# Kernel tuning notes

Hardware: AMD Instinct MI355X
Metric: run time of the kernel (lower is better)

Reference implementation:

```python
import jax, jax.numpy as jnp
import numpy as np

H, C, HID, NLAYERS, B = 4, 32, 128, 3, 2048
EPS = 1e-5


def _gat_layer(x, src, dst, n, W, b, a_src, a_dst):
    # x: [N, HID]; W: [HID, H*C]; a_src/a_dst: [H, C]
    h = (x @ W).reshape(n, H, C)                      # [N,H,C]
    s_src = jnp.einsum('nhc,hc->nh', h, a_src)        # [N,H]
    s_dst = jnp.einsum('nhc,hc->nh', h, a_dst)
    e = jax.nn.leaky_relu(s_src[src] + s_dst[dst], 0.2)   # [E,H]
    m = jax.ops.segment_max(e, dst, num_segments=n)
    p = jnp.exp(e - m[dst])
    z = jax.ops.segment_sum(p, dst, num_segments=n)
    alpha = p / z[dst]                                 # scatter-softmax over in-edges
    msg = h[src] * alpha[:, :, None]                   # [E,H,C]
    out = jax.ops.segment_sum(msg, dst, num_segments=n)
    return out.reshape(n, H * C) + b


def _layernorm(x, g, bta):
    mu = jnp.mean(x, axis=-1, keepdims=True)
    var = jnp.mean(jnp.square(x - mu), axis=-1, keepdims=True)
    return (x - mu) * jax.lax.rsqrt(var + EPS) * g + bta


def _encode(x, edge_index, batch, W_in, b_in, Wg, bg, att_src, att_dst, ln_gamma, ln_beta):
    n = x.shape[0]
    # add self loops (PyG GATConv default)
    loops = jnp.arange(n, dtype=edge_index.dtype)
    src = jnp.concatenate([edge_index[0], loops])
    dst = jnp.concatenate([edge_index[1], loops])
    h = jax.nn.relu(x @ W_in + b_in)
    for i in range(NLAYERS):
        res = h
        h = _gat_layer(h, src, dst, n, Wg[i], bg[i], att_src[i], att_dst[i])
        h = _layernorm(h, ln_gamma[i], ln_beta[i])
        h = jax.nn.relu(h)
        h = h + res
    # global mean pool
    sums = jax.ops.segment_sum(h, batch, num_segments=B)
    cnt = jax.ops.segment_sum(jnp.ones((n,), h.dtype), batch, num_segments=B)
    return sums / jnp.maximum(cnt, 1.0)[:, None]


def setup_inputs() -> dict:
    key = jax.random.key(0)
    ks = jax.random.split(key, 24)
    Nt, Et, Np, Ep, D = 131072, 2097152, 24576, 196608, 480
    inp = {}
    inp['tcr_x'] = jax.random.normal(ks[0], (Nt, D), jnp.float32)
    inp['tcr_edge_index'] = jax.random.randint(ks[1], (2, Et), 0, Nt)
    inp['tcr_batch'] = jnp.sort(jax.random.randint(ks[2], (Nt,), 0, B))
    inp['pep_x'] = jax.random.normal(ks[3], (Np, D), jnp.float32)
    inp['pep_edge_index'] = jax.random.randint(ks[4], (2, Ep), 0, Np)
    inp['pep_batch'] = jnp.sort(jax.random.randint(ks[5], (Np,), 0, B))
    s_in = 1.0 / np.sqrt(D)
    inp['W_in'] = jax.random.normal(ks[6], (D, HID), jnp.float32) * s_in
    inp['b_in'] = jnp.zeros((HID,), jnp.float32)
    s_h = 1.0 / np.sqrt(HID)
    inp['Wg'] = jax.random.normal(ks[7], (NLAYERS, HID, H * C), jnp.float32) * s_h
    inp['bg'] = jnp.zeros((NLAYERS, HID), jnp.float32)
    inp['att_src'] = jax.random.normal(ks[8], (NLAYERS, H, C), jnp.float32) * (1.0 / np.sqrt(C))
    inp['att_dst'] = jax.random.normal(ks[9], (NLAYERS, H, C), jnp.float32) * (1.0 / np.sqrt(C))
    inp['ln_gamma'] = jnp.ones((NLAYERS, HID), jnp.float32)
    inp['ln_beta'] = jnp.zeros((NLAYERS, HID), jnp.float32)
    inp['Wc1'] = jax.random.normal(ks[10], (2 * HID, HID), jnp.float32) * (1.0 / np.sqrt(2 * HID))
    inp['bc1'] = jnp.zeros((HID,), jnp.float32)
    inp['Wc2'] = jax.random.normal(ks[11], (HID, HID // 2), jnp.float32) * s_h
    inp['bc2'] = jnp.zeros((HID // 2,), jnp.float32)
    inp['Wc3'] = jax.random.normal(ks[12], (HID // 2, 1), jnp.float32) * (1.0 / np.sqrt(HID // 2))
    inp['bc3'] = jnp.zeros((1,), jnp.float32)
    return inp


def reference(tcr_x, tcr_edge_index, tcr_batch, pep_x, pep_edge_index, pep_batch,
              W_in, b_in, Wg, bg, att_src, att_dst, ln_gamma, ln_beta,
              Wc1, bc1, Wc2, bc2, Wc3, bc3):
    tcr = _encode(tcr_x, tcr_edge_index, tcr_batch, W_in, b_in, Wg, bg, att_src, att_dst, ln_gamma, ln_beta)
    pep = _encode(pep_x, pep_edge_index, pep_batch, W_in, b_in, Wg, bg, att_src, att_dst, ln_gamma, ln_beta)
    z = jnp.concatenate([tcr, pep], axis=1)            # [B, 256]
    z = jax.nn.relu(z @ Wc1 + bc1)
    z = jax.nn.relu(z @ Wc2 + bc2)
    return jax.nn.sigmoid(z @ Wc3 + bc3)               # [B, 1]
```

## Files before the change

### kernel.cpp

```cpp
#include <hip/hip_runtime.h>
#include <hip/hip_fp16.h>
#include <math.h>

#define NHEAD   4
#define CDIM    32
#define HIDDIM  128
#define NLAYERS 3
#define DIN     480
#define LN_EPS  1e-5f
#define NSPLIT  4

typedef _Float16 f16x8 __attribute__((ext_vector_type(8)));
typedef float    f32x4 __attribute__((ext_vector_type(4)));
typedef int      int4u __attribute__((ext_vector_type(4), aligned(4)));

__global__ void hist_kernel(const int* __restrict__ tei, const int* __restrict__ pei,
                            int* __restrict__ deg, int Et, int Ep, int Nt, int N) {
    int i = blockIdx.x * 256 + threadIdx.x;
    int tot = Et + Ep + N;
    if (i >= tot) return;
    int d;
    if (i < Et)            d = tei[Et + i];
    else if (i < Et + Ep)  d = pei[Ep + (i - Et)] + Nt;
    else                   d = i - Et - Ep;
    atomicAdd(&deg[d], 1);
}

__global__ __launch_bounds__(256) void fill_kernel(const int* __restrict__ tei,
                                                   const int* __restrict__ pei,
                                                   int* __restrict__ cursor,
                                                   int* __restrict__ col,
                                                   int Et, int Ep, int Nt, int N,
                                                   float oscale) {
    int oid    = blockIdx.x & (NSPLIT - 1);
    int chunk  = blockIdx.x / NSPLIT;
    int nchunk = gridDim.x / NSPLIT;
    int tot = Et + Ep + N;
    int per = (tot + nchunk - 1) / nchunk;
    int e0 = chunk * per;
    int e1 = min(e0 + per, tot);
    for (int i = e0 + (int)threadIdx.x; i < e1; i += 256) {
        int d;
        bool self = false;
        if (i < Et)           d = tei[Et + i];
        else if (i < Et + Ep) d = pei[Ep + (i - Et)] + Nt;
        else                { d = i - Et - Ep; self = true; }
        int owner = (int)((float)d * oscale);
        owner = owner > NSPLIT - 1 ? NSPLIT - 1 : owner;
        if (owner != oid) continue;
        int s;
        if (self)        s = d;
        else if (i < Et) s = tei[i];
        else             s = pei[i - Et] + Nt;
        int pos = atomicAdd(&cursor[d], 1);
        col[pos] = s;
    }
}

__global__ __launch_bounds__(256) void scan_reduce(const int* __restrict__ deg,
                                                   int* __restrict__ part, int N) {
    __shared__ int sm[256];
    int t = threadIdx.x;
    int base = blockIdx.x * 1024 + t * 4;
    int4 v = make_int4(0, 0, 0, 0);
    if (base + 3 < N) v = *(const int4*)(deg + base);
    else if (base < N) {
        v.x = deg[base];
        if (base + 1 < N) v.y = deg[base + 1];
        if (base + 2 < N) v.z = deg[base + 2];
    }
    sm[t] = v.x + v.y + v.z + v.w;
    __syncthreads();
    for (int off = 128; off >= 1; off >>= 1) {
        if (t < off) sm[t] += sm[t + off];
        __syncthreads();
    }
    if (t == 0) part[blockIdx.x] = sm[0];
}

__global__ __launch_bounds__(256) void scan_partials(int* __restrict__ part,
                                                     int* __restrict__ rowptr,
                                                     int npart, int N) {
    __shared__ int sm[256];
    int t = threadIdx.x;
    sm[t] = (t < npart) ? part[t] : 0;
    __syncthreads();
    for (int off = 1; off < 256; off <<= 1) {
        int u = (t >= off) ? sm[t - off] : 0;
        __syncthreads();
        sm[t] += u;
        __syncthreads();
    }
    if (t < npart) part[t] = (t == 0) ? 0 : sm[t - 1];
    if (t == 0) rowptr[N] = sm[255];
}

__global__ __launch_bounds__(256) void scan_final(const int* __restrict__ deg,
                                                  const int* __restrict__ part,
                                                  int* __restrict__ rowptr,
                                                  int* __restrict__ cursor, int N) {
    __shared__ int sm[256];
    int t = threadIdx.x;
    int base = blockIdx.x * 1024 + t * 4;
    int4 v = make_int4(0, 0, 0, 0);
    if (base + 3 < N) v = *(const int4*)(deg + base);
    else if (base < N) {
        v.x = deg[base];
        if (base + 1 < N) v.y = deg[base + 1];
        if (base + 2 < N) v.z = deg[base + 2];
    }
    sm[t] = v.x + v.y + v.z + v.w;
    __syncthreads();
    for (int off = 1; off < 256; off <<= 1) {
        int u = (t >= off) ? sm[t - off] : 0;
        __syncthreads();
        sm[t] += u;
        __syncthreads();
    }
    int run = ((t == 0) ? 0 : sm[t - 1]) + part[blockIdx.x];
    if (base < N)     { rowptr[base]     = run; cursor[base]     = run; run += v.x; }
    if (base + 1 < N) { rowptr[base + 1] = run; cursor[base + 1] = run; run += v.y; }
    if (base + 2 < N) { rowptr[base + 2] = run; cursor[base + 2] = run; run += v.z; }
    if (base + 3 < N) { rowptr[base + 3] = run; cursor[base + 3] = run; }
}

__global__ void transpose_w(const float* __restrict__ W, _Float16* __restrict__ Wt,
                            int K) {
    int idx = blockIdx.x * 256 + threadIdx.x;
    if (idx >= K * 128) return;
    int n = idx / K, k = idx - n * K;
    Wt[idx] = (_Float16)W[(size_t)k * 128 + n];
}

#define ASTRIDE 40

template<int OUT_F16>
__global__ __launch_bounds__(256) void mfma_gemm(const float* __restrict__ A,
                                                 const _Float16* __restrict__ Wt,
                                                 const float* __restrict__ bias,
                                                 void* __restrict__ Cout,
                                                 const float* __restrict__ a_src,
                                                 const float* __restrict__ a_dst,
                                                 float* __restrict__ ssrc,
                                                 float* __restrict__ sdst,
                                                 int K) {
    __shared__ _Float16 As[64 * ASTRIDE];
    __shared__ _Float16 Ws[128 * ASTRIDE];
    const int tid  = threadIdx.x;
    const int bn   = blockIdx.x * 64;
    const int wave = tid >> 6, lane = tid & 63;
    const int lm   = lane & 15, q = lane >> 4;

    f32x4 acc[8];
#pragma unroll
    for (int i = 0; i < 8; ++i) acc[i] = (f32x4){0.f, 0.f, 0.f, 0.f};

    for (int kt = 0; kt < K; kt += 32) {
#pragma unroll
        for (int p = 0; p < 2; ++p) {
            int f  = p * 256 + tid;
            int r  = f >> 3;
            int c4 = (f & 7) * 4;
            float4 v = *(const float4*)(A + (size_t)(bn + r) * K + kt + c4);
            _Float16* d = &As[r * ASTRIDE + c4];
            d[0] = (_Float16)v.x; d[1] = (_Float16)v.y;
            d[2] = (_Float16)v.z; d[3] = (_Float16)v.w;
        }
#pragma unroll
        for (int p = 0; p < 2; ++p) {
            int f   = p * 256 + tid;
            int n   = f >> 2;
            int seg = (f & 3) * 8;
            *(float4*)(&Ws[n * ASTRIDE + seg]) =
                *(const float4*)(Wt + (size_t)n * K + kt + seg);
        }
        __syncthreads();
        f16x8 af = *(const f16x8*)(&As[(wave * 16 + lm) * ASTRIDE + q * 8]);
#pragma unroll
        for (int nt = 0; nt < 8; ++nt) {
            f16x8 bf = *(const f16x8*)(&Ws[(nt * 16 + lm) * ASTRIDE + q * 8]);
            acc[nt] = __builtin_amdgcn_mfma_f32_16x16x32_f16(af, bf, acc[nt], 0, 0, 0);
        }
        __syncthreads();
    }

    const int row0 = bn + wave * 16 + q * 4;
    if (OUT_F16) {
        _Float16* C = (_Float16*)Cout;
        float as[8], ad[8];
#pragma unroll
        for (int nt = 0; nt < 8; ++nt) {
            as[nt] = a_src[nt * 16 + lm];
            ad[nt] = a_dst[nt * 16 + lm];
        }
        float myS = 0.f, myD = 0.f;
#pragma unroll
        for (int i = 0; i < 4; ++i) {
            float ps[4], pd[4];
#pragma unroll
            for (int h = 0; h < 4; ++h) {
                ps[h] = as[2 * h] * acc[2 * h][i] + as[2 * h + 1] * acc[2 * h + 1][i];
                pd[h] = ad[2 * h] * acc[2 * h][i] + ad[2 * h + 1] * acc[2 * h + 1][i];
            }
#pragma unroll
            for (int k = 1; k < 16; k <<= 1) {
#pragma unroll
                for (int h = 0; h < 4; ++h) {
                    ps[h] += __shfl_xor(ps[h], k, 16);
                    pd[h] += __shfl_xor(pd[h], k, 16);
                }
            }
            if ((lm >> 2) == i) { myS = ps[lm & 3]; myD = pd[lm & 3]; }
#pragma unroll
            for (int nt = 0; nt < 8; ++nt)
                C[(size_t)(row0 + i) * 128 + nt * 16 + lm] = (_Float16)acc[nt][i];
        }
        int sr = (row0 + (lm >> 2)) * 4 + (lm & 3);
        ssrc[sr] = myS;
        sdst[sr] = myD;
    } else {
        float* C = (float*)Cout;
#pragma unroll
        for (int nt = 0; nt < 8; ++nt) {
            int c = nt * 16 + lm;
            float bv = bias[c];
#pragma unroll
            for (int i = 0; i < 4; ++i)
                C[(size_t)(row0 + i) * 128 + c] = fmaxf(acc[nt][i] + bv, 0.f);
        }
    }
}

__global__ __launch_bounds__(256) void gather_kernel(const f16x8* __restrict__ h2v,
                                                     const float* __restrict__ ssrc,
                                                     const float* __restrict__ sdst,
                                                     const int* __restrict__ rowptr,
                                                     const int* __restrict__ col,
                                                     const float* __restrict__ bg,
                                                     const float* __restrict__ gamma,
                                                     const float* __restrict__ beta,
                                                     float* __restrict__ hio, int N) {
    int wave = threadIdx.x >> 6, lane = threadIdx.x & 63;
    int g = lane >> 4, t = lane & 15;
    int n = blockIdx.x * 16 + wave * 4 + g;
    bool valid = n < N;
    int nn = valid ? n : 0;
    int head = t >> 2;
    int beg = rowptr[nn];
    int end = valid ? rowptr[nn + 1] : beg;
    float sd = sdst[nn * 4 + head];

    float m = -1e30f, z = 0.f;
    float a[8];
#pragma unroll
    for (int k = 0; k < 8; ++k) a[k] = 0.f;

    int j = beg;
    for (; j + 3 < end; j += 4) {
        int4u cv = *(const int4u*)(col + j);
        int s0 = cv.x, s1 = cv.y, s2 = cv.z, s3 = cv.w;
        float e0 = ssrc[s0 * 4 + head] + sd;
        float e1 = ssrc[s1 * 4 + head] + sd;
        float e2 = ssrc[s2 * 4 + head] + sd;
        float e3 = ssrc[s3 * 4 + head] + sd;
        f16x8 v0 = h2v[(size_t)s0 * 16 + t];
        f16x8 v1 = h2v[(size_t)s1 * 16 + t];
        f16x8 v2 = h2v[(size_t)s2 * 16 + t];
        f16x8 v3 = h2v[(size_t)s3 * 16 + t];
        e0 = fmaxf(e0, 0.2f * e0);
        e1 = fmaxf(e1, 0.2f * e1);
        e2 = fmaxf(e2, 0.2f * e2);
        e3 = fmaxf(e3, 0.2f * e3);
        float nm = fmaxf(fmaxf(fmaxf(e0, e1), fmaxf(e2, e3)), m);
        float r  = __expf(m - nm);
        m = nm;
        float p0 = __expf(e0 - nm);
        float p1 = __expf(e1 - nm);
        float p2 = __expf(e2 - nm);
        float p3 = __expf(e3 - nm);
        z = z * r + (p0 + p1 + p2 + p3);
#pragma unroll
        for (int k = 0; k < 8; ++k) a[k] *= r;
#pragma unroll
        for (int k = 0; k < 8; ++k) a[k] = fmaf((float)v0[k], p0, a[k]);
#pragma unroll
        for (int k = 0; k < 8; ++k) a[k] = fmaf((float)v1[k], p1, a[k]);
#pragma unroll
        for (int k = 0; k < 8; ++k) a[k] = fmaf((float)v2[k], p2, a[k]);
#pragma unroll
        for (int k = 0; k < 8; ++k) a[k] = fmaf((float)v3[k], p3, a[k]);
    }
    for (; j < end; ++j) {
        int s = col[j];
        float e = ssrc[s * 4 + head] + sd;
        e = fmaxf(e, 0.2f * e);
        f16x8 v = h2v[(size_t)s * 16 + t];
        float nm = fmaxf(m, e);
        float r  = __expf(m - nm);
        float p  = __expf(e - nm);
        m = nm;
        z = z * r + p;
#pragma unroll
        for (int k = 0; k < 8; ++k) a[k] = fmaf((float)v[k], p, a[k] * r);
    }

    if (!valid) return;
    float inv = 1.f / z;
    int c0 = t * 8;
    float4 bgv0 = *(const float4*)(bg + c0);
    float4 bgv1 = *(const float4*)(bg + c0 + 4);
    float o[8];
    o[0] = a[0] * inv + bgv0.x; o[1] = a[1] * inv + bgv0.y;
    o[2] = a[2] * inv + bgv0.z; o[3] = a[3] * inv + bgv0.w;
    o[4] = a[4] * inv + bgv1.x; o[5] = a[5] * inv + bgv1.y;
    o[6] = a[6] * inv + bgv1.z; o[7] = a[7] * inv + bgv1.w;
    float s = 0.f;
#pragma unroll
    for (int k = 0; k < 8; ++k) s += o[k];
#pragma unroll
    for (int k = 1; k < 16; k <<= 1) s += __shfl_xor(s, k, 16);
    float mu = s * (1.f / 128.f);
    float q = 0.f;
#pragma unroll
    for (int k = 0; k < 8; ++k) q += (o[k] - mu) * (o[k] - mu);
#pragma unroll
    for (int k = 1; k < 16; k <<= 1) q += __shfl_xor(q, k, 16);
    float rs = rsqrtf(q * (1.f / 128.f) + LN_EPS);
    float4 gm0 = *(const float4*)(gamma + c0);
    float4 gm1 = *(const float4*)(gamma + c0 + 4);
    float4 bt0 = *(const float4*)(beta + c0);
    float4 bt1 = *(const float4*)(beta + c0 + 4);
    float* hrow = hio + (size_t)n * 128 + c0;
    float4 r0 = *(const float4*)(hrow);
    float4 r1 = *(const float4*)(hrow + 4);
    float4 y0, y1;
    y0.x = fmaxf((o[0] - mu) * rs * gm0.x + bt0.x, 0.f) + r0.x;
    y0.y = fmaxf((o[1] - mu) * rs * gm0.y + bt0.y, 0.f) + r0.y;
    y0.z = fmaxf((o[2] - mu) * rs * gm0.z + bt0.z, 0.f) + r0.z;
    y0.w = fmaxf((o[3] - mu) * rs * gm0.w + bt0.w, 0.f) + r0.w;
    y1.x = fmaxf((o[4] - mu) * rs * gm1.x + bt1.x, 0.f) + r1.x;
    y1.y = fmaxf((o[5] - mu) * rs * gm1.y + bt1.y, 0.f) + r1.y;
    y1.z = fmaxf((o[6] - mu) * rs * gm1.z + bt1.z, 0.f) + r1.z;
    y1.w = fmaxf((o[7] - mu) * rs * gm1.w + bt1.w, 0.f) + r1.w;
    *(float4*)(hrow)     = y0;
    *(float4*)(hrow + 4) = y1;
}

__global__ __launch_bounds__(128) void pool_kernel(const float* __restrict__ h,
                                                   const int* __restrict__ tb,
                                                   const int* __restrict__ pb,
                                                   float* __restrict__ pooled,
                                                   int Nt, int Np, int B) {
    int blk = blockIdx.x;
    bool is_t = blk < B;
    int bb = is_t ? blk : blk - B;
    const int* __restrict__ arr = is_t ? tb : pb;
    int len  = is_t ? Nt : Np;
    int base = is_t ? 0 : Nt;
    int off  = is_t ? 0 : 128;
    int lo = 0, hi = len;
    while (lo < hi) { int mid = (lo + hi) >> 1; if (arr[mid] < bb) lo = mid + 1; else hi = mid; }
    int beg = lo;
    hi = len;
    while (lo < hi) { int mid = (lo + hi) >> 1; if (arr[mid] < bb + 1) lo = mid + 1; else hi = mid; }
    int end = lo;
    int t = threadIdx.x;
    float a0 = 0.f, a1 = 0.f, a2 = 0.f, a3 = 0.f;
    int n = beg;
    for (; n + 3 < end; n += 4) {
        a0 += h[(size_t)(base + n)     * 128 + t];
        a1 += h[(size_t)(base + n + 1) * 128 + t];
        a2 += h[(size_t)(base + n + 2) * 128 + t];
        a3 += h[(size_t)(base + n + 3) * 128 + t];
    }
    for (; n < end; ++n) a0 += h[(size_t)(base + n) * 128 + t];
    float s = (a0 + a1) + (a2 + a3);
    float invc = 1.f / (float)max(end - beg, 1);
    pooled[(size_t)bb * 256 + off + t] = s * invc;
}

__global__ __launch_bounds__(128) void classifier_kernel(const float* __restrict__ pooled,
                                                         const float* __restrict__ Wc1,
                                                         const float* __restrict__ bc1,
                                                         const float* __restrict__ Wc2,
                                                         const float* __restrict__ bc2,
                                                         const float* __restrict__ Wc3,
                                                         const float* __restrict__ bc3,
                                                         float* __restrict__ outp, int B) {
    __shared__ float z[256];
    __shared__ float a1[128];
    __shared__ float a2[64];
    int r = blockIdx.x, t = threadIdx.x;
    z[t]       = pooled[(size_t)r * 256 + t];
    z[128 + t] = pooled[(size_t)r * 256 + 128 + t];
    __syncthreads();
    float acc = bc1[t];
    for (int k = 0; k < 256; ++k) acc = fmaf(z[k], Wc1[k * 128 + t], acc);
    a1[t] = fmaxf(acc, 0.f);
    __syncthreads();
    if (t < 64) {
        float a = bc2[t];
        for (int k = 0; k < 128; ++k) a = fmaf(a1[k], Wc2[k * 64 + t], a);
        a2[t] = fmaxf(a, 0.f);
    }
    __syncthreads();
    if (t < 64) {
        float p = a2[t] * Wc3[t];
#pragma unroll
        for (int k = 1; k < 64; k <<= 1) p += __shfl_xor(p, k);
        if (t == 0) outp[r] = 1.f / (1.f + __expf(-(p + bc3[0])));
    }
}

extern "C" void kernel_launch(void* const* d_in, const int* in_sizes, int n_in,
                              void* d_out, int out_size, void* d_ws, size_t ws_size,
                              hipStream_t stream) {
    const float* tcr_x     = (const float*)d_in[0];
    const int*   tcr_ei    = (const int*)d_in[1];
    const int*   tcr_batch = (const int*)d_in[2];
    const float* pep_x     = (const float*)d_in[3];
    const int*   pep_ei    = (const int*)d_in[4];
    const int*   pep_batch = (const int*)d_in[5];
    const float* W_in      = (const float*)d_in[6];
    const float* b_in      = (const float*)d_in[7];
    const float* Wg        = (const float*)d_in[8];
    const float* bg        = (const float*)d_in[9];
    const float* att_src   = (const float*)d_in[10];
    const float* att_dst   = (const float*)d_in[11];
    const float* ln_gamma  = (const float*)d_in[12];
    const float* ln_beta   = (const float*)d_in[13];
    const float* Wc1       = (const float*)d_in[14];
    const float* bc1       = (const float*)d_in[15];
    const float* Wc2       = (const float*)d_in[16];
    const float* bc2       = (const float*)d_in[17];
    const float* Wc3       = (const float*)d_in[18];
    const float* bc3       = (const float*)d_in[19];

    const int Nt = in_sizes[0] / DIN;
    const int Et = in_sizes[1] / 2;
    const int Np = in_sizes[3] / DIN;
    const int Ep = in_sizes[4] / 2;
    const int B  = out_size;
    const int N  = Nt + Np;
    const int Etot = Et + Ep + N;

    char* w = (char*)d_ws;
    size_t o = 0;
    auto alloc = [&](size_t bytes) -> char* {
        size_t r = (o + 255) & ~(size_t)255;
        o = r + bytes;
        return w + r;
    };
    float*    pooled = (float*)alloc((size_t)B * 256 * 4);
    float*    h_a    = (float*)alloc((size_t)N * 128 * 4);
    _Float16* h2h    = (_Float16*)alloc((size_t)N * 128 * 2);
    _Float16* WtIn   = (_Float16*)alloc((size_t)128 * DIN * 2);
    _Float16* WtG    = (_Float16*)alloc((size_t)NLAYERS * 128 * 128 * 2);
    float*    ssrc   = (float*)alloc((size_t)N * 4 * 4);
    float*    sdst   = (float*)alloc((size_t)N * 4 * 4);
    int* rowptr      = (int*)alloc((size_t)(N + 1) * 4);
    int* cursor      = (int*)alloc((size_t)N * 4);
    int* deg         = (int*)alloc((size_t)N * 4);
    int* part        = (int*)alloc(256 * 4);
    int* col         = (int*)alloc((size_t)Etot * 4);
    (void)ws_size; (void)n_in;

    hipMemsetAsync(deg, 0, (size_t)N * 4, stream);

    transpose_w<<<(128 * DIN + 255) / 256, 256, 0, stream>>>(W_in, WtIn, DIN);
    for (int i = 0; i < NLAYERS; ++i)
        transpose_w<<<(128 * 128 + 255) / 256, 256, 0, stream>>>(
            Wg + (size_t)i * HIDDIM * HIDDIM, WtG + (size_t)i * 128 * 128, 128);

    hist_kernel<<<(Etot + 255) / 256, 256, 0, stream>>>(tcr_ei, pep_ei, deg, Et, Ep, Nt, N);
    int nblk = (N + 1023) / 1024;
    scan_reduce<<<nblk, 256, 0, stream>>>(deg, part, N);
    scan_partials<<<1, 256, 0, stream>>>(part, rowptr, nblk, N);
    scan_final<<<nblk, 256, 0, stream>>>(deg, part, rowptr, cursor, N);
    fill_kernel<<<NSPLIT * 512, 256, 0, stream>>>(tcr_ei, pep_ei, cursor, col,
                                                  Et, Ep, Nt, N, (float)NSPLIT / (float)N);

    mfma_gemm<0><<<Nt / 64, 256, 0, stream>>>(tcr_x, WtIn, b_in, h_a,
                                              nullptr, nullptr, nullptr, nullptr, DIN);
    mfma_gemm<0><<<Np / 64, 256, 0, stream>>>(pep_x, WtIn, b_in, h_a + (size_t)Nt * 128,
                                              nullptr, nullptr, nullptr, nullptr, DIN);

    for (int i = 0; i < NLAYERS; ++i) {
        mfma_gemm<1><<<N / 64, 256, 0, stream>>>(h_a, WtG + (size_t)i * 128 * 128,
                                                 nullptr, h2h,
                                                 att_src + i * NHEAD * CDIM,
                                                 att_dst + i * NHEAD * CDIM,
                                                 ssrc, sdst, 128);
        gather_kernel<<<(N + 15) / 16, 256, 0, stream>>>((const f16x8*)h2h, ssrc, sdst,
                                                         rowptr, col, bg + i * HIDDIM,
                                                         ln_gamma + i * HIDDIM,
                                                         ln_beta + i * HIDDIM, h_a, N);
    }
    pool_kernel<<<2 * B, 128, 0, stream>>>(h_a, tcr_batch, pep_batch, pooled, Nt, Np, B);

    classifier_kernel<<<B, 128, 0, stream>>>(pooled, Wc1, bc1, Wc2, bc2,
                                             Wc3, bc3, (float*)d_out, B);
}
```

Measured before the change: 1.148 ms.

## Merge launches and software-pipeline gather loads in GAT aggregation

After: 1.149 ms. No clear change (+0.1%).

```diff
diff --git a/kernel.cpp b/kernel.cpp
--- a/kernel.cpp
+++ b/kernel.cpp
@@ -124,18 +124,31 @@
     if (base + 3 < N) { rowptr[base + 3] = run; cursor[base + 3] = run; }
 }
 
-__global__ void transpose_w(const float* __restrict__ W, _Float16* __restrict__ Wt,
-                            int K) {
+__global__ __launch_bounds__(256) void transpose_all(const float* __restrict__ W_in,
+                                                     const float* __restrict__ Wg,
+                                                     _Float16* __restrict__ WtIn,
+                                                     _Float16* __restrict__ WtG) {
     int idx = blockIdx.x * 256 + threadIdx.x;
-    if (idx >= K * 128) return;
-    int n = idx / K, k = idx - n * K;
-    Wt[idx] = (_Float16)W[(size_t)k * 128 + n];
+    const int NIN = 128 * DIN;
+    if (idx < NIN) {
+        int n = idx / DIN, k = idx - n * DIN;
+        WtIn[idx] = (_Float16)W_in[(size_t)k * 128 + n];
+    } else {
+        int r = idx - NIN;
+        if (r >= NLAYERS * 128 * 128) return;
+        int l = r / (128 * 128), rr = r - l * 128 * 128;
+        int n = rr >> 7, k = rr & 127;
+        WtG[(size_t)l * 128 * 128 + rr] =
+            (_Float16)Wg[(size_t)l * 128 * 128 + (size_t)k * 128 + n];
+    }
 }
 
 #define ASTRIDE 40
 
 template<int OUT_F16>
 __global__ __launch_bounds__(256) void mfma_gemm(const float* __restrict__ A,
+                                                 const float* __restrict__ A2,
+                                                 int NtRows,
                                                  const _Float16* __restrict__ Wt,
                                                  const float* __restrict__ bias,
                                                  void* __restrict__ Cout,
@@ -151,6 +164,11 @@
     const int wave = tid >> 6, lane = tid & 63;
     const int lm   = lane & 15, q = lane >> 4;
 
+    const float* __restrict__ Abase;
+    int arow;
+    if (A2 && bn >= NtRows) { Abase = A2; arow = bn - NtRows; }
+    else                    { Abase = A;  arow = bn; }
+
     f32x4 acc[8];
 #pragma unroll
     for (int i = 0; i < 8; ++i) acc[i] = (f32x4){0.f, 0.f, 0.f, 0.f};
@@ -161,7 +179,7 @@
             int f  = p * 256 + tid;
             int r  = f >> 3;
             int c4 = (f & 7) * 4;
-            float4 v = *(const float4*)(A + (size_t)(bn + r) * K + kt + c4);
+            float4 v = *(const float4*)(Abase + (size_t)(arow + r) * K + kt + c4);
             _Float16* d = &As[r * ASTRIDE + c4];
             d[0] = (_Float16)v.x; d[1] = (_Float16)v.y;
             d[2] = (_Float16)v.z; d[3] = (_Float16)v.w;
@@ -255,22 +273,12 @@
 #pragma unroll
     for (int k = 0; k < 8; ++k) a[k] = 0.f;
 
-    int j = beg;
-    for (; j + 3 < end; j += 4) {
-        int4u cv = *(const int4u*)(col + j);
-        int s0 = cv.x, s1 = cv.y, s2 = cv.z, s3 = cv.w;
-        float e0 = ssrc[s0 * 4 + head] + sd;
-        float e1 = ssrc[s1 * 4 + head] + sd;
-        float e2 = ssrc[s2 * 4 + head] + sd;
-        float e3 = ssrc[s3 * 4 + head] + sd;
-        f16x8 v0 = h2v[(size_t)s0 * 16 + t];
-        f16x8 v1 = h2v[(size_t)s1 * 16 + t];
-        f16x8 v2 = h2v[(size_t)s2 * 16 + t];
-        f16x8 v3 = h2v[(size_t)s3 * 16 + t];
-        e0 = fmaxf(e0, 0.2f * e0);
-        e1 = fmaxf(e1, 0.2f * e1);
-        e2 = fmaxf(e2, 0.2f * e2);
-        e3 = fmaxf(e3, 0.2f * e3);
+    auto compute4 = [&](f16x8 v0, f16x8 v1, f16x8 v2, f16x8 v3,
+                        float x0, float x1, float x2, float x3) {
+        float e0 = x0 + sd; e0 = fmaxf(e0, 0.2f * e0);
+        float e1 = x1 + sd; e1 = fmaxf(e1, 0.2f * e1);
+        float e2 = x2 + sd; e2 = fmaxf(e2, 0.2f * e2);
+        float e3 = x3 + sd; e3 = fmaxf(e3, 0.2f * e3);
         float nm = fmaxf(fmaxf(fmaxf(e0, e1), fmaxf(e2, e3)), m);
         float r  = __expf(m - nm);
         m = nm;
@@ -289,6 +297,37 @@
         for (int k = 0; k < 8; ++k) a[k] = fmaf((float)v2[k], p2, a[k]);
 #pragma unroll
         for (int k = 0; k < 8; ++k) a[k] = fmaf((float)v3[k], p3, a[k]);
+    };
+
+    int j = beg;
+    int nch = (end - beg) >> 2;
+    if (nch > 0) {
+        int4u cv = *(const int4u*)(col + j);
+        f16x8 v0 = h2v[(size_t)cv.x * 16 + t];
+        f16x8 v1 = h2v[(size_t)cv.y * 16 + t];
+        f16x8 v2 = h2v[(size_t)cv.z * 16 + t];
+        f16x8 v3 = h2v[(size_t)cv.w * 16 + t];
+        float x0 = ssrc[cv.x * 4 + head];
+        float x1 = ssrc[cv.y * 4 + head];
+        float x2 = ssrc[cv.z * 4 + head];
+        float x3 = ssrc[cv.w * 4 + head];
+        for (int c = 1; c < nch; ++c) {
+            j += 4;
+            int4u cn = *(const int4u*)(col + j);
+            f16x8 w0 = h2v[(size_t)cn.x * 16 + t];
+            f16x8 w1 = h2v[(size_t)cn.y * 16 + t];
+            f16x8 w2 = h2v[(size_t)cn.z * 16 + t];
+            f16x8 w3 = h2v[(size_t)cn.w * 16 + t];
+            float u0 = ssrc[cn.x * 4 + head];
+            float u1 = ssrc[cn.y * 4 + head];
+            float u2 = ssrc[cn.z * 4 + head];
+            float u3 = ssrc[cn.w * 4 + head];
+            compute4(v0, v1, v2, v3, x0, x1, x2, x3);
+            v0 = w0; v1 = w1; v2 = w2; v3 = w3;
+            x0 = u0; x1 = u1; x2 = u2; x3 = u3;
+        }
+        compute4(v0, v1, v2, v3, x0, x1, x2, x3);
+        j += 4;
     }
     for (; j < end; ++j) {
         int s = col[j];
@@ -346,53 +385,55 @@
     *(float4*)(hrow + 4) = y1;
 }
 
-__global__ __launch_bounds__(128) void pool_kernel(const float* __restrict__ h,
-                                                   const int* __restrict__ tb,
-                                                   const int* __restrict__ pb,
-                                                   float* __restrict__ pooled,
-                                                   int Nt, int Np, int B) {
-    int blk = blockIdx.x;
-    bool is_t = blk < B;
-    int bb = is_t ? blk : blk - B;
-    const int* __restrict__ arr = is_t ? tb : pb;
-    int len  = is_t ? Nt : Np;
-    int base = is_t ? 0 : Nt;
-    int off  = is_t ? 0 : 128;
-    int lo = 0, hi = len;
-    while (lo < hi) { int mid = (lo + hi) >> 1; if (arr[mid] < bb) lo = mid + 1; else hi = mid; }
-    int beg = lo;
-    hi = len;
-    while (lo < hi) { int mid = (lo + hi) >> 1; if (arr[mid] < bb + 1) lo = mid + 1; else hi = mid; }
-    int end = lo;
-    int t = threadIdx.x;
-    float a0 = 0.f, a1 = 0.f, a2 = 0.f, a3 = 0.f;
-    int n = beg;
-    for (; n + 3 < end; n += 4) {
-        a0 += h[(size_t)(base + n)     * 128 + t];
-        a1 += h[(size_t)(base + n + 1) * 128 + t];
-        a2 += h[(size_t)(base + n + 2) * 128 + t];
-        a3 += h[(size_t)(base + n + 3) * 128 + t];
-    }
-    for (; n < end; ++n) a0 += h[(size_t)(base + n) * 128 + t];
-    float s = (a0 + a1) + (a2 + a3);
-    float invc = 1.f / (float)max(end - beg, 1);
-    pooled[(size_t)bb * 256 + off + t] = s * invc;
-}
-
-__global__ __launch_bounds__(128) void classifier_kernel(const float* __restrict__ pooled,
-                                                         const float* __restrict__ Wc1,
-                                                         const float* __restrict__ bc1,
-                                                         const float* __restrict__ Wc2,
-                                                         const float* __restrict__ bc2,
-                                                         const float* __restrict__ Wc3,
-                                                         const float* __restrict__ bc3,
-                                                         float* __restrict__ outp, int B) {
+__global__ __launch_bounds__(128) void pool_classifier_kernel(
+        const float* __restrict__ h,
+        const int* __restrict__ tb, const int* __restrict__ pb,
+        const float* __restrict__ Wc1, const float* __restrict__ bc1,
+        const float* __restrict__ Wc2, const float* __restrict__ bc2,
+        const float* __restrict__ Wc3, const float* __restrict__ bc3,
+        float* __restrict__ outp, int Nt, int Np, int B) {
     __shared__ float z[256];
     __shared__ float a1[128];
     __shared__ float a2[64];
     int r = blockIdx.x, t = threadIdx.x;
-    z[t]       = pooled[(size_t)r * 256 + t];
-    z[128 + t] = pooled[(size_t)r * 256 + 128 + t];
+    {
+        int lo = 0, hi = Nt;
+        while (lo < hi) { int mid = (lo + hi) >> 1; if (tb[mid] < r) lo = mid + 1; else hi = mid; }
+        int beg = lo;
+        hi = Nt;
+        while (lo < hi) { int mid = (lo + hi) >> 1; if (tb[mid] < r + 1) lo = mid + 1; else hi = mid; }
+        int end = lo;
+        float s0 = 0.f, s1 = 0.f, s2 = 0.f, s3 = 0.f;
+        int n = beg;
+        for (; n + 3 < end; n += 4) {
+            s0 += h[(size_t)n * 128 + t];
+            s1 += h[(size_t)(n + 1) * 128 + t];
+            s2 += h[(size_t)(n + 2) * 128 + t];
+            s3 += h[(size_t)(n + 3) * 128 + t];
+        }
+        for (; n < end; ++n) s0 += h[(size_t)n * 128 + t];
+        float invc = 1.f / (float)max(end - beg, 1);
+        z[t] = ((s0 + s1) + (s2 + s3)) * invc;
+    }
+    {
+        int lo = 0, hi = Np;
+        while (lo < hi) { int mid = (lo + hi) >> 1; if (pb[mid] < r) lo = mid + 1; else hi = mid; }
+        int beg = lo;
+        hi = Np;
+        while (lo < hi) { int mid = (lo + hi) >> 1; if (pb[mid] < r + 1) lo = mid + 1; else hi = mid; }
+        int end = lo;
+        float s0 = 0.f, s1 = 0.f, s2 = 0.f, s3 = 0.f;
+        int n = beg;
+        for (; n + 3 < end; n += 4) {
+            s0 += h[(size_t)(Nt + n) * 128 + t];
+            s1 += h[(size_t)(Nt + n + 1) * 128 + t];
+            s2 += h[(size_t)(Nt + n + 2) * 128 + t];
+            s3 += h[(size_t)(Nt + n + 3) * 128 + t];
+        }
+        for (; n < end; ++n) s0 += h[(size_t)(Nt + n) * 128 + t];
+        float invc = 1.f / (float)max(end - beg, 1);
+        z[128 + t] = ((s0 + s1) + (s2 + s3)) * invc;
+    }
     __syncthreads();
     float acc = bc1[t];
     for (int k = 0; k < 256; ++k) acc = fmaf(z[k], Wc1[k * 128 + t], acc);
@@ -451,7 +492,6 @@
         o = r + bytes;
         return w + r;
     };
-    float*    pooled = (float*)alloc((size_t)B * 256 * 4);
     float*    h_a    = (float*)alloc((size_t)N * 128 * 4);
     _Float16* h2h    = (_Float16*)alloc((size_t)N * 128 * 2);
     _Float16* WtIn   = (_Float16*)alloc((size_t)128 * DIN * 2);
@@ -467,10 +507,8 @@
 
     hipMemsetAsync(deg, 0, (size_t)N * 4, stream);
 
-    transpose_w<<<(128 * DIN + 255) / 256, 256, 0, stream>>>(W_in, WtIn, DIN);
-    for (int i = 0; i < NLAYERS; ++i)
-        transpose_w<<<(128 * 128 + 255) / 256, 256, 0, stream>>>(
-            Wg + (size_t)i * HIDDIM * HIDDIM, WtG + (size_t)i * 128 * 128, 128);
+    transpose_all<<<(128 * DIN + NLAYERS * 128 * 128 + 255) / 256, 256, 0, stream>>>(
+        W_in, Wg, WtIn, WtG);
 
     hist_kernel<<<(Etot + 255) / 256, 256, 0, stream>>>(tcr_ei, pep_ei, deg, Et, Ep, Nt, N);
     int nblk = (N + 1023) / 1024;
@@ -480,13 +518,12 @@
     fill_kernel<<<NSPLIT * 512, 256, 0, stream>>>(tcr_ei, pep_ei, cursor, col,
                                                   Et, Ep, Nt, N, (float)NSPLIT / (float)N);
 
-    mfma_gemm<0><<<Nt / 64, 256, 0, stream>>>(tcr_x, WtIn, b_in, h_a,
-                                              nullptr, nullptr, nullptr, nullptr, DIN);
-    mfma_gemm<0><<<Np / 64, 256, 0, stream>>>(pep_x, WtIn, b_in, h_a + (size_t)Nt * 128,
-                                              nullptr, nullptr, nullptr, nullptr, DIN);
+    mfma_gemm<0><<<N / 64, 256, 0, stream>>>(tcr_x, pep_x, Nt, WtIn, b_in, h_a,
+                                             nullptr, nullptr, nullptr, nullptr, DIN);
 
     for (int i = 0; i < NLAYERS; ++i) {
-        mfma_gemm<1><<<N / 64, 256, 0, stream>>>(h_a, WtG + (size_t)i * 128 * 128,
+        mfma_gemm<1><<<N / 64, 256, 0, stream>>>(h_a, nullptr, 0x40000000,
+                                                 WtG + (size_t)i * 128 * 128,
                                                  nullptr, h2h,
                                                  att_src + i * NHEAD * CDIM,
                                                  att_dst + i * NHEAD * CDIM,
@@ -496,8 +533,7 @@
                                                          ln_gamma + i * HIDDIM,
                                                          ln_beta + i * HIDDIM, h_a, N);
     }
-    pool_kernel<<<2 * B, 128, 0, stream>>>(h_a, tcr_batch, pep_batch, pooled, Nt, Np, B);
-
-    classifier_kernel<<<B, 128, 0, stream>>>(pooled, Wc1, bc1, Wc2, bc2,
-                                             Wc3, bc3, (float*)d_out, B);
-}
+    pool_classifier_kernel<<<B, 128, 0, stream>>>(h_a, tcr_batch, pep_batch,
+                                                  Wc1, bc1, Wc2, bc2, Wc3, bc3,
+                                                  (float*)d_out, Nt, Np, B);
+}
```
